# Kernel optimization log

Hardware: AMD Instinct MI355X
Metric: run time of the kernel (lower is better)

## Reference

```python
import jax, jax.numpy as jnp
import numpy as np

DEPTH = 4      # number of VSS blocks
C = 256        # channels / d_inner (expansion_factor=1)
DS = 16        # d_state
DTR = 16       # dt_rank = ceil(C/16)
BATCH, DD, HH, WW = 2, 16, 16, 16


def _ln(x, g, b, eps=1e-5):
    m = jnp.mean(x, -1, keepdims=True)
    v = jnp.var(x, -1, keepdims=True)
    return (x - m) * jax.lax.rsqrt(v + eps) * g + b


def _silu(x):
    return x * jax.nn.sigmoid(x)


def _block(x, ori, p):
    # x: [B,H,W,Dp,C] channel-last volume tokens
    B, H, W, Dp, Cd = x.shape
    L = H * W * Dp
    h = _ln(x, p['ln1_g'], p['ln1_b'])
    xz = h @ p['in_w'].T                       # [B,H,W,Dp,2C]
    xs, z = jnp.split(xz, 2, axis=-1)
    xc = jnp.transpose(xs, (0, 4, 1, 2, 3))    # [B,C,H,W,Dp]
    xc = jax.lax.conv_general_dilated(
        xc, p['conv_w'], (1, 1, 1), 'SAME',
        dimension_numbers=('NCDHW', 'OIDHW', 'NCDHW'),
        feature_group_count=Cd) + p['conv_b'][None, :, None, None, None]
    xc = _silu(xc)
    # orientation: 3 bits flip the spatial axes before raster flatten
    flip_axes = tuple(ax for bit, ax in ((1, 2), (2, 3), (4, 4)) if ori & bit)
    if flip_axes:
        xc = jnp.flip(xc, flip_axes)
    seq = xc.reshape(B, Cd, L).transpose(0, 2, 1)   # [B,L,C]
    dbl = seq @ p['xproj_w'].T                       # [B,L,DTR+2*DS]
    dt, Bm, Cm = dbl[..., :DTR], dbl[..., DTR:DTR + DS], dbl[..., DTR + DS:]
    dt = jax.nn.softplus(dt @ p['dt_w'].T + p['dt_b'])   # [B,L,C]
    A = -jnp.exp(p['A_log'])                              # [C,DS]
    dA = jnp.exp(dt[..., None] * A)                       # [B,L,C,DS]
    dBx = dt[..., None] * Bm[:, :, None, :] * seq[..., None]

    def step(carry, inp):
        dA_t, dBx_t, C_t = inp
        carry = dA_t * carry + dBx_t                      # [B,C,DS]
        y = jnp.einsum('bdn,bn->bd', carry, C_t)
        return carry, y

    h0 = jnp.zeros((B, Cd, DS), dA.dtype)
    _, ys = jax.lax.scan(step, h0, (dA.transpose(1, 0, 2, 3),
                                    dBx.transpose(1, 0, 2, 3),
                                    Cm.transpose(1, 0, 2)))
    y = ys.transpose(1, 0, 2) + p['D'] * seq              # [B,L,C]
    yv = y.transpose(0, 2, 1).reshape(B, Cd, H, W, Dp)
    if flip_axes:
        yv = jnp.flip(yv, flip_axes)
    y = jnp.transpose(yv, (0, 2, 3, 4, 1))                # [B,H,W,Dp,C]
    y = _ln(y, p['on_g'], p['on_b'])
    y = y * _silu(z)
    return x + y @ p['out_w'].T


def setup_inputs() -> dict:
    key = jax.random.key(0)
    ks = jax.random.split(key, 12)
    d = {}
    d['x'] = jax.random.normal(ks[0], (BATCH, C, DD, HH, WW), jnp.float32)
    d['in_w'] = jax.random.normal(ks[1], (DEPTH, 2 * C, C), jnp.float32) * 0.02
    d['conv_w'] = jax.random.normal(ks[2], (DEPTH, C, 1, 3, 3, 3), jnp.float32) * 0.1
    d['conv_b'] = jnp.zeros((DEPTH, C), jnp.float32)
    d['xproj_w'] = jax.random.normal(ks[3], (DEPTH, DTR + 2 * DS, C), jnp.float32) * 0.02
    d['dt_w'] = jax.random.normal(ks[4], (DEPTH, C, DTR), jnp.float32) * 0.02
    d['dt_b'] = jax.random.uniform(ks[5], (DEPTH, C), jnp.float32, -4.0, -2.0)
    # S4D-real init for A_log
    d['A_log'] = jnp.tile(jnp.log(jnp.arange(1, DS + 1, dtype=jnp.float32))[None, None, :], (DEPTH, C, 1))
    d['D_skip'] = jnp.ones((DEPTH, C), jnp.float32)
    d['on_g'] = jnp.ones((DEPTH, C), jnp.float32)
    d['on_b'] = jnp.zeros((DEPTH, C), jnp.float32)
    d['out_w'] = jax.random.normal(ks[6], (DEPTH, C, C), jnp.float32) * 0.02
    d['ln1_g'] = jnp.ones((DEPTH, C), jnp.float32)
    d['ln1_b'] = jnp.zeros((DEPTH, C), jnp.float32)
    d['post_g'] = jnp.ones((C,), jnp.float32)
    d['post_b'] = jnp.zeros((C,), jnp.float32)
    return d


def reference(x, in_w, conv_w, conv_b, xproj_w, dt_w, dt_b, A_log, D_skip,
              on_g, on_b, out_w, ln1_g, ln1_b, post_g, post_b):
    # [B,C,D,H,W] -> [B,H,W,D,C]
    t = jnp.transpose(x, (0, 3, 4, 2, 1))
    for i in range(DEPTH):
        p = dict(in_w=in_w[i], conv_w=conv_w[i], conv_b=conv_b[i],
                 xproj_w=xproj_w[i], dt_w=dt_w[i], dt_b=dt_b[i],
                 A_log=A_log[i], D=D_skip[i], on_g=on_g[i], on_b=on_b[i],
                 out_w=out_w[i], ln1_g=ln1_g[i], ln1_b=ln1_b[i])
        t = _block(t, i % 8, p)
    t = _ln(t, post_g, post_b)
    # [B,H,W,D,C] -> [B,C,D,H,W]
    return jnp.transpose(t, (0, 4, 3, 1, 2))
```

## Files before the change

kernel.cpp:

```cpp
#include <hip/hip_runtime.h>
#include <math.h>

#define B_ 2
#define C_ 256
#define L_ 4096
#define BL_ 8192
#define DEPTH_ 4
#define CK_ 64
#define CL_ 64

typedef __attribute__((ext_vector_type(8))) short bf16x8;
typedef __attribute__((ext_vector_type(4))) float f32x4;
#define MFMA16 __builtin_amdgcn_mfma_f32_16x16x32_bf16

__device__ __forceinline__ float silu_(float x){ return x/(1.f+__expf(-x)); }
__device__ __forceinline__ float softplus_(float x){ return fmaxf(x,0.f)+log1pf(__expf(-fabsf(x))); }
__device__ __forceinline__ unsigned short f2b_(float f){
    union{float f;unsigned u;}v; v.f=f;
    unsigned r=(v.u + 0x7fffu + ((v.u>>16)&1u))>>16;
    return (unsigned short)r;
}
__device__ __forceinline__ float b2f_(unsigned short u){
    union{unsigned u;float f;}v; v.u=((unsigned)u)<<16; return v.f;
}

__global__ __launch_bounds__(256) void k_w2b(const float* __restrict__ src, unsigned short* __restrict__ dst)
{
    int i=blockIdx.x*256+threadIdx.x;
    float4 v=((const float4*)src)[i];
    ushort4 o; o.x=f2b_(v.x); o.y=f2b_(v.y); o.z=f2b_(v.z); o.w=f2b_(v.w);
    ((ushort4*)dst)[i]=o;
}

__global__ __launch_bounds__(256) void k_wdt(
    const float* __restrict__ dtw, const float* __restrict__ xw,
    unsigned short* __restrict__ wdtb)
{
    int blk=blockIdx.x;
    int i=blk>>8, c=blk&255, k=threadIdx.x;
    const float* dr=dtw+((size_t)i*C_+c)*16;
    const float* xr=xw+(size_t)i*48*C_+k;
    float acc=0.f;
    #pragma unroll
    for(int j=0;j<16;j++) acc=fmaf(dr[j], xr[(size_t)j*C_], acc);
    wdtb[((size_t)i*C_+c)*C_+k]=f2b_(acc);
}

__global__ __launch_bounds__(256) void k_t_in(const float* __restrict__ x, float* __restrict__ t)
{
    __shared__ float tile[16*257];
    int blk=blockIdx.x, b=blk>>8, d=(blk>>4)&15, h=blk&15;
    int tid=threadIdx.x;
    int w2=tid&15;
    for(int p=0;p<16;p++){
        int c=(tid>>4)+16*p;
        tile[w2*257+c]=x[((size_t)(b*C_+c))*4096 + d*256 + h*16 + w2];
    }
    __syncthreads();
    for(int k=0;k<16;k++){
        t[((size_t)b*L_+(h*16+k)*16+d)*C_+tid]=tile[k*257+tid];
    }
}

__global__ __launch_bounds__(256) void k_ln(
    const float* __restrict__ t, const float* __restrict__ g,
    const float* __restrict__ be, unsigned short* __restrict__ hb)
{
    int wv=threadIdx.x>>6, lane=threadIdx.x&63;
    int row=blockIdx.x*4+wv;
    float4 v=((const float4*)(t+(size_t)row*C_))[lane];
    float s=v.x+v.y+v.z+v.w;
    float ss=v.x*v.x+v.y*v.y+v.z*v.z+v.w*v.w;
    #pragma unroll
    for(int m=1;m<64;m<<=1){ s+=__shfl_xor(s,m); ss+=__shfl_xor(ss,m); }
    float mn=s*(1.f/256.f);
    float rs=rsqrtf(ss*(1.f/256.f)-mn*mn+1e-5f);
    float4 gg=((const float4*)g)[lane];
    float4 bb=((const float4*)be)[lane];
    ushort4 o;
    o.x=f2b_((v.x-mn)*rs*gg.x+bb.x);
    o.y=f2b_((v.y-mn)*rs*gg.y+bb.y);
    o.z=f2b_((v.z-mn)*rs*gg.z+bb.z);
    o.w=f2b_((v.w-mn)*rs*gg.w+bb.w);
    ((ushort4*)(hb+(size_t)row*C_))[lane]=o;
}

__global__ __launch_bounds__(256) void k_gemm_in(
    const unsigned short* __restrict__ Ab, const unsigned short* __restrict__ Wb,
    float* __restrict__ xs, float* __restrict__ z)
{
    int wv=threadIdx.x>>6, lane=threadIdx.x&63;
    int m0=blockIdx.x*64+(wv>>1)*32;
    int n0=blockIdx.y*64+(wv&1)*32;
    int la=lane&15, kg=lane>>4;
    f32x4 acc[2][2];
    #pragma unroll
    for(int i=0;i<2;i++)
        #pragma unroll
        for(int j=0;j<2;j++) acc[i][j]=(f32x4){0.f,0.f,0.f,0.f};
    const unsigned short* a0p=Ab+(size_t)(m0+la)*C_+kg*8;
    const unsigned short* a1p=Ab+(size_t)(m0+16+la)*C_+kg*8;
    const unsigned short* b0p=Wb+(size_t)(n0+la)*C_+kg*8;
    const unsigned short* b1p=Wb+(size_t)(n0+16+la)*C_+kg*8;
    #pragma unroll
    for(int kk=0;kk<C_;kk+=32){
        bf16x8 a0=*(const bf16x8*)(a0p+kk);
        bf16x8 a1=*(const bf16x8*)(a1p+kk);
        bf16x8 b0=*(const bf16x8*)(b0p+kk);
        bf16x8 b1=*(const bf16x8*)(b1p+kk);
        acc[0][0]=MFMA16(a0,b0,acc[0][0],0,0,0);
        acc[0][1]=MFMA16(a0,b1,acc[0][1],0,0,0);
        acc[1][0]=MFMA16(a1,b0,acc[1][0],0,0,0);
        acc[1][1]=MFMA16(a1,b1,acc[1][1],0,0,0);
    }
    #pragma unroll
    for(int mi=0;mi<2;mi++)
        #pragma unroll
        for(int nj=0;nj<2;nj++)
            #pragma unroll
            for(int r=0;r<4;r++){
                int m=m0+mi*16+kg*4+r;
                int n=n0+nj*16+la;
                float val=acc[mi][nj][r];
                if(n<256) xs[(size_t)m*C_+n]=val;
                else      z [(size_t)m*C_+(n-256)]=val;
            }
}

__global__ __launch_bounds__(256) void k_gemm_out(
    const unsigned short* __restrict__ Ab, const unsigned short* __restrict__ Wb,
    float* __restrict__ t)
{
    int wv=threadIdx.x>>6, lane=threadIdx.x&63;
    int m0=blockIdx.x*64+(wv>>1)*32;
    int n0=blockIdx.y*64+(wv&1)*32;
    int la=lane&15, kg=lane>>4;
    f32x4 acc[2][2];
    #pragma unroll
    for(int i=0;i<2;i++)
        #pragma unroll
        for(int j=0;j<2;j++) acc[i][j]=(f32x4){0.f,0.f,0.f,0.f};
    const unsigned short* a0p=Ab+(size_t)(m0+la)*C_+kg*8;
    const unsigned short* a1p=Ab+(size_t)(m0+16+la)*C_+kg*8;
    const unsigned short* b0p=Wb+(size_t)(n0+la)*C_+kg*8;
    const unsigned short* b1p=Wb+(size_t)(n0+16+la)*C_+kg*8;
    #pragma unroll
    for(int kk=0;kk<C_;kk+=32){
        bf16x8 a0=*(const bf16x8*)(a0p+kk);
        bf16x8 a1=*(const bf16x8*)(a1p+kk);
        bf16x8 b0=*(const bf16x8*)(b0p+kk);
        bf16x8 b1=*(const bf16x8*)(b1p+kk);
        acc[0][0]=MFMA16(a0,b0,acc[0][0],0,0,0);
        acc[0][1]=MFMA16(a0,b1,acc[0][1],0,0,0);
        acc[1][0]=MFMA16(a1,b0,acc[1][0],0,0,0);
        acc[1][1]=MFMA16(a1,b1,acc[1][1],0,0,0);
    }
    #pragma unroll
    for(int mi=0;mi<2;mi++)
        #pragma unroll
        for(int nj=0;nj<2;nj++)
            #pragma unroll
            for(int r=0;r<4;r++){
                int m=m0+mi*16+kg*4+r;
                int n=n0+nj*16+la;
                float* tp=t+(size_t)m*C_+n;
                *tp=*tp+acc[mi][nj][r];
            }
}

__global__ __launch_bounds__(256) void k_gemm_xdt(
    const unsigned short* __restrict__ Ab, const unsigned short* __restrict__ Wxb,
    const unsigned short* __restrict__ Wdtb, const float* __restrict__ dtbias,
    float* __restrict__ BC, float* __restrict__ dt)
{
    int by=blockIdx.y;
    int wv=threadIdx.x>>6, lane=threadIdx.x&63;
    int la=lane&15, kg=lane>>4;
    f32x4 acc[2][2];
    #pragma unroll
    for(int i=0;i<2;i++)
        #pragma unroll
        for(int j=0;j<2;j++) acc[i][j]=(f32x4){0.f,0.f,0.f,0.f};
    if(by==4){
        if(blockIdx.x>=64) return;
        int m0=blockIdx.x*128+wv*32;
        const unsigned short* a0p=Ab+(size_t)(m0+la)*C_+kg*8;
        const unsigned short* a1p=Ab+(size_t)(m0+16+la)*C_+kg*8;
        const unsigned short* b0p=Wxb+(size_t)(16+la)*C_+kg*8;
        const unsigned short* b1p=Wxb+(size_t)(32+la)*C_+kg*8;
        #pragma unroll
        for(int kk=0;kk<C_;kk+=32){
            bf16x8 a0=*(const bf16x8*)(a0p+kk);
            bf16x8 a1=*(const bf16x8*)(a1p+kk);
            bf16x8 b0=*(const bf16x8*)(b0p+kk);
            bf16x8 b1=*(const bf16x8*)(b1p+kk);
            acc[0][0]=MFMA16(a0,b0,acc[0][0],0,0,0);
            acc[0][1]=MFMA16(a0,b1,acc[0][1],0,0,0);
            acc[1][0]=MFMA16(a1,b0,acc[1][0],0,0,0);
            acc[1][1]=MFMA16(a1,b1,acc[1][1],0,0,0);
        }
        #pragma unroll
        for(int mi=0;mi<2;mi++)
            #pragma unroll
            for(int nj=0;nj<2;nj++)
                #pragma unroll
                for(int r=0;r<4;r++){
                    int m=m0+mi*16+kg*4+r;
                    BC[(size_t)m*32 + nj*16+la]=acc[mi][nj][r];
                }
    } else {
        int m0=blockIdx.x*64+(wv>>1)*32;
        int n0=by*64+(wv&1)*32;
        const unsigned short* a0p=Ab+(size_t)(m0+la)*C_+kg*8;
        const unsigned short* a1p=Ab+(size_t)(m0+16+la)*C_+kg*8;
        const unsigned short* b0p=Wdtb+(size_t)(n0+la)*C_+kg*8;
        const unsigned short* b1p=Wdtb+(size_t)(n0+16+la)*C_+kg*8;
        #pragma unroll
        for(int kk=0;kk<C_;kk+=32){
            bf16x8 a0=*(const bf16x8*)(a0p+kk);
            bf16x8 a1=*(const bf16x8*)(a1p+kk);
            bf16x8 b0=*(const bf16x8*)(b0p+kk);
            bf16x8 b1=*(const bf16x8*)(b1p+kk);
            acc[0][0]=MFMA16(a0,b0,acc[0][0],0,0,0);
            acc[0][1]=MFMA16(a0,b1,acc[0][1],0,0,0);
            acc[1][0]=MFMA16(a1,b0,acc[1][0],0,0,0);
            acc[1][1]=MFMA16(a1,b1,acc[1][1],0,0,0);
        }
        float bias0=dtbias[n0+la], bias1=dtbias[n0+16+la];
        #pragma unroll
        for(int mi=0;mi<2;mi++)
            #pragma unroll
            for(int nj=0;nj<2;nj++)
                #pragma unroll
                for(int r=0;r<4;r++){
                    int m=m0+mi*16+kg*4+r;
                    int n=n0+nj*16+la;
                    float val=acc[mi][nj][r]+((nj==0)?bias0:bias1);
                    dt[(size_t)m*C_+n]=softplus_(val);
                }
    }
}

__global__ __launch_bounds__(256) void k_conv(
    const float* __restrict__ xs, const float* __restrict__ cw,
    const float* __restrict__ cb, unsigned short* __restrict__ seqb, int ori)
{
    __shared__ float wl[256*27];
    int tid=threadIdx.x;
    for(int j=tid;j<256*27;j+=256) wl[j]=cw[j];
    int blk=blockIdx.x;
    int b=blk>>8, h=(blk>>4)&15, w=blk&15;
    __syncthreads();
    const float* wp=wl+tid*27;
    float bias=cb[tid];
    float acc[16];
    #pragma unroll
    for(int d=0;d<16;d++) acc[d]=bias;
    #pragma unroll
    for(int kh=0;kh<3;kh++){
        int hh=h+kh-1; if((unsigned)hh>=16u) continue;
        #pragma unroll
        for(int kw=0;kw<3;kw++){
            int ww=w+kw-1; if((unsigned)ww>=16u) continue;
            const float* bp=xs+((size_t)(b*L_)+(hh*16+ww)*16)*C_+tid;
            float w0=wp[(kh*3+kw)*3+0];
            float w1=wp[(kh*3+kw)*3+1];
            float w2=wp[(kh*3+kw)*3+2];
            #pragma unroll
            for(int dd=0;dd<16;dd++){
                float v=bp[(size_t)dd*C_];
                if(dd<15) acc[dd+1]=fmaf(w0,v,acc[dd+1]);
                acc[dd]=fmaf(w1,v,acc[dd]);
                if(dd>0)  acc[dd-1]=fmaf(w2,v,acc[dd-1]);
            }
        }
    }
    int hf=(ori&1)?15-h:h;
    int wf=(ori&2)?15-w:w;
    size_t obase=((size_t)b*L_+(hf*16+wf)*16)*C_+tid;
    #pragma unroll
    for(int d=0;d<16;d++){
        float a=silu_(acc[d]);
        int df=(ori&4)?15-d:d;
        seqb[obase+(size_t)df*C_]=f2b_(a);
    }
}

__global__ __launch_bounds__(256) void k_scan1(
    const unsigned short* __restrict__ seqb, const float* __restrict__ dtlc,
    const float* __restrict__ BC, const float* __restrict__ A_log,
    float* __restrict__ Ap, float* __restrict__ Ho)
{
    __shared__ float2 dxL[64][17];
    __shared__ float  bcL[64][16];
    int tid=threadIdx.x;
    int blk=blockIdx.x, cg=blk>>6, ck=blk&63;
    int p0=cg*16, b=p0>>8, c0=p0&255;
    int l0=ck*CL_;
    {
        int lr=tid>>2, c4=tid&3;
        size_t base=((size_t)(b*L_+l0+lr))*C_ + c0 + c4*4;
        ushort4 xu=*(const ushort4*)(seqb+base);
        float4 d4=*(const float4*)(dtlc+base);
        dxL[lr][c4*4+0]=make_float2(d4.x,b2f_(xu.x));
        dxL[lr][c4*4+1]=make_float2(d4.y,b2f_(xu.y));
        dxL[lr][c4*4+2]=make_float2(d4.z,b2f_(xu.z));
        dxL[lr][c4*4+3]=make_float2(d4.w,b2f_(xu.w));
        if(c4==0){
            const float* bs=BC+((size_t)(b*L_+l0+lr))*32;
            float4 bv0=*(const float4*)bs, bv1=*(const float4*)(bs+4);
            float4 bv2=*(const float4*)(bs+8), bv3=*(const float4*)(bs+12);
            *(float4*)&bcL[lr][0]=bv0;  *(float4*)&bcL[lr][4]=bv1;
            *(float4*)&bcL[lr][8]=bv2;  *(float4*)&bcL[lr][12]=bv3;
        }
    }
    __syncthreads();
    int wv=tid>>6, lane=tid&63, grp=lane>>4, n=lane&15;
    int cl=wv*4+grp, pair=p0+cl, c=c0+cl;
    float An=-__expf(A_log[c*16+n]);
    float carry=0.f, sdt=0.f;
    #pragma unroll 8
    for(int l=0;l<CL_;l++){
        float2 dx=dxL[l][cl];
        float bv=bcL[l][n];
        float dA=__expf(dx.x*An);
        carry=fmaf(dA,carry,dx.x*bv*dx.y);
        sdt+=dx.x;
    }
    int idx=(pair*CK_+ck)*16+n;
    Ap[idx]=__expf(An*sdt); Ho[idx]=carry;
}

__global__ __launch_bounds__(256) void k_scan2(
    const float* __restrict__ Ap, const float* __restrict__ Ho, float* __restrict__ Sb)
{
    int gid=blockIdx.x*256+threadIdx.x;
    int pair=gid>>4, n=gid&15;
    float S=0.f;
    #pragma unroll
    for(int ck=0;ck<CK_;ck++){
        int idx=(pair*CK_+ck)*16+n;
        Sb[idx]=S;
        S=fmaf(Ap[idx],S,Ho[idx]);
    }
}

__global__ __launch_bounds__(256) void k_scan3(
    const unsigned short* __restrict__ seqb, const float* __restrict__ dtlc,
    const float* __restrict__ BC, const float* __restrict__ A_log,
    const float* __restrict__ Dsk, const float* __restrict__ Sb,
    float* __restrict__ y)
{
    __shared__ float2 dxL[64][17];
    __shared__ float  bcL[64][32];
    __shared__ float  sc[16][16][17];
    int tid=threadIdx.x;
    int blk=blockIdx.x, cg=blk>>6, ck=blk&63;
    int p0=cg*16, b=p0>>8, c0=p0&255;
    int l0=ck*CL_;
    {
        int lr=tid>>2, c4=tid&3;
        size_t base=((size_t)(b*L_+l0+lr))*C_ + c0 + c4*4;
        ushort4 xu=*(const ushort4*)(seqb+base);
        float4 d4=*(const float4*)(dtlc+base);
        dxL[lr][c4*4+0]=make_float2(d4.x,b2f_(xu.x));
        dxL[lr][c4*4+1]=make_float2(d4.y,b2f_(xu.y));
        dxL[lr][c4*4+2]=make_float2(d4.z,b2f_(xu.z));
        dxL[lr][c4*4+3]=make_float2(d4.w,b2f_(xu.w));
        const float* bs=BC+((size_t)(b*L_+l0+lr))*32 + c4*8;
        float4 bv0=*(const float4*)bs, bv1=*(const float4*)(bs+4);
        *(float4*)&bcL[lr][c4*8]=bv0;
        *(float4*)&bcL[lr][c4*8+4]=bv1;
    }
    __syncthreads();
    int wv=tid>>6, lane=tid&63, grp=lane>>4, n=lane&15;
    int cl=wv*4+grp, pair=p0+cl, c=c0+cl;
    float An=-__expf(A_log[c*16+n]);
    float Dc=Dsk[c];
    float carry=Sb[(pair*CK_+ck)*16+n];
    float ybuf[4], xsv[4];
    #pragma unroll
    for(int q=0;q<4;q++){
        float parts[16];
        #pragma unroll
        for(int l2=0;l2<16;l2++){
            int l=q*16+l2;
            float2 dx=dxL[l][cl];
            float bv=bcL[l][n];
            float cv=bcL[l][16+n];
            float dA=__expf(dx.x*An);
            carry=fmaf(dA,carry,dx.x*bv*dx.y);
            parts[l2]=carry*cv;
            if(l2==n) xsv[q]=dx.y;
        }
        #pragma unroll
        for(int l2=0;l2<16;l2++) sc[cl][l2][n]=parts[l2];
        __syncthreads();
        float s=0.f;
        #pragma unroll
        for(int n2=0;n2<16;n2++) s+=sc[cl][n][n2];
        ybuf[q]=fmaf(Dc,xsv[q],s);
        __syncthreads();
    }
    float* yT=(float*)&sc[0][0][0];
    #pragma unroll
    for(int q=0;q<4;q++){
        int l=q*16+n;
        yT[l*17+cl]=ybuf[q];
    }
    __syncthreads();
    {
        int lr=tid>>2, c4=tid&3;
        size_t base=((size_t)(b*L_+l0+lr))*C_ + c0 + c4*4;
        float4 o=make_float4(yT[lr*17+c4*4+0],yT[lr*17+c4*4+1],
                             yT[lr*17+c4*4+2],yT[lr*17+c4*4+3]);
        *(float4*)(y+base)=o;
    }
}

__global__ __launch_bounds__(256) void k_post(
    const float* __restrict__ y, const float* __restrict__ z,
    const float* __restrict__ og, const float* __restrict__ ob,
    unsigned short* __restrict__ y2b, int ori)
{
    int wv=threadIdx.x>>6, lane=threadIdx.x&63;
    int row=blockIdx.x*4+wv;
    int b=row>>12, l=row&4095;
    int d=l&15, w=(l>>4)&15, h=l>>8;
    int hf=(ori&1)?15-h:h, wf=(ori&2)?15-w:w, df=(ori&4)?15-d:d;
    int lf=(hf*16+wf)*16+df;
    float4 v=((const float4*)(y+((size_t)b*L_+lf)*C_))[lane];
    float s=v.x+v.y+v.z+v.w;
    float ss=v.x*v.x+v.y*v.y+v.z*v.z+v.w*v.w;
    #pragma unroll
    for(int m=1;m<64;m<<=1){ s+=__shfl_xor(s,m); ss+=__shfl_xor(ss,m); }
    float mn=s*(1.f/256.f);
    float rstd=rsqrtf(ss*(1.f/256.f)-mn*mn+1e-5f);
    float4 gg=((const float4*)og)[lane];
    float4 bb=((const float4*)ob)[lane];
    float4 zv=((const float4*)(z+((size_t)b*L_+l)*C_))[lane];
    ushort4 o;
    o.x=f2b_(((v.x-mn)*rstd*gg.x+bb.x)*silu_(zv.x));
    o.y=f2b_(((v.y-mn)*rstd*gg.y+bb.y)*silu_(zv.y));
    o.z=f2b_(((v.z-mn)*rstd*gg.z+bb.z)*silu_(zv.z));
    o.w=f2b_(((v.w-mn)*rstd*gg.w+bb.w)*silu_(zv.w));
    ((ushort4*)(y2b+((size_t)b*L_+l)*C_))[lane]=o;
}

__global__ __launch_bounds__(256) void k_final(
    const float* __restrict__ t, const float* __restrict__ pg,
    const float* __restrict__ pb, float* __restrict__ out)
{
    __shared__ float tile[16*257];
    __shared__ float mrs[16][2];
    int blk=blockIdx.x, b=blk>>8, d=(blk>>4)&15, h=blk&15;
    int tid=threadIdx.x;
    for(int w2=0;w2<16;w2++){
        tile[w2*257+tid]=t[((size_t)b*L_+(h*16+w2)*16+d)*C_+tid];
    }
    __syncthreads();
    int r=tid>>4, p=tid&15;
    float s=0.f, ss=0.f;
    #pragma unroll
    for(int k=0;k<16;k++){ float v=tile[r*257+k*16+p]; s+=v; ss+=v*v; }
    #pragma unroll
    for(int m=1;m<16;m<<=1){ s+=__shfl_xor(s,m); ss+=__shfl_xor(ss,m); }
    if(p==0){ float mn=s*(1.f/256.f); mrs[r][0]=mn; mrs[r][1]=rsqrtf(ss*(1.f/256.f)-mn*mn+1e-5f); }
    __syncthreads();
    int w2=tid&15;
    for(int p2=0;p2<16;p2++){
        int c=(tid>>4)+16*p2;
        float v=tile[w2*257+c];
        float vn=(v-mrs[w2][0])*mrs[w2][1]*pg[c]+pb[c];
        out[((size_t)(b*C_+c))*4096 + d*256 + h*16 + w2]=vn;
    }
}

extern "C" void kernel_launch(void* const* d_in, const int* in_sizes, int n_in,
                              void* d_out, int out_size, void* d_ws, size_t ws_size,
                              hipStream_t stream)
{
    (void)in_sizes; (void)n_in; (void)out_size; (void)ws_size;
    const float* x      =(const float*)d_in[0];
    const float* in_w   =(const float*)d_in[1];
    const float* conv_w =(const float*)d_in[2];
    const float* conv_b =(const float*)d_in[3];
    const float* xproj_w=(const float*)d_in[4];
    const float* dt_w   =(const float*)d_in[5];
    const float* dt_b   =(const float*)d_in[6];
    const float* A_log  =(const float*)d_in[7];
    const float* D_skip =(const float*)d_in[8];
    const float* on_g   =(const float*)d_in[9];
    const float* on_b   =(const float*)d_in[10];
    const float* out_w  =(const float*)d_in[11];
    const float* ln1_g  =(const float*)d_in[12];
    const float* ln1_b  =(const float*)d_in[13];
    const float* post_g =(const float*)d_in[14];
    const float* post_b =(const float*)d_in[15];
    float* out=(float*)d_out;
    float* ws=(float*)d_ws;

    const size_t NBL=(size_t)BL_*C_;
    float* t    = ws;
    float* xs   = ws +   NBL;
    float* z    = ws + 2*NBL;
    float* seq  = ws + 3*NBL;
    float* BC   = ws + 4*NBL;
    float* Ap   = BC + (size_t)BL_*32;
    float* Ho   = Ap + 512*CK_*16;
    float* Sb   = Ho + 512*CK_*16;
    unsigned short* hb   = (unsigned short*)(Sb + 512*CK_*16);
    unsigned short* seqb = hb   + NBL;
    unsigned short* y2b  = seqb + NBL;
    unsigned short* wbI  = y2b  + NBL;
    unsigned short* wbO  = wbI + (size_t)DEPTH_*512*C_;
    unsigned short* xwb  = wbO + (size_t)DEPTH_*C_*C_;
    unsigned short* wdtb = xwb + (size_t)DEPTH_*48*C_;
    float* dtlc = xs;

    k_w2b<<<DEPTH_*512*C_/1024,256,0,stream>>>(in_w, wbI);
    k_w2b<<<DEPTH_*C_*C_/1024,256,0,stream>>>(out_w, wbO);
    k_w2b<<<DEPTH_*48*C_/1024,256,0,stream>>>(xproj_w, xwb);
    k_wdt<<<DEPTH_*C_,256,0,stream>>>(dt_w, xproj_w, wdtb);
    k_t_in<<<512,256,0,stream>>>(x,t);
    for(int i=0;i<DEPTH_;i++){
        int ori=i&7;
        k_ln<<<2048,256,0,stream>>>(t, ln1_g+i*256, ln1_b+i*256, hb);
        k_gemm_in<<<dim3(128,8),256,0,stream>>>(hb, wbI+(size_t)i*512*C_, xs, z);
        k_conv<<<512,256,0,stream>>>(xs, conv_w+(size_t)i*6912, conv_b+i*256, seqb, ori);
        k_gemm_xdt<<<dim3(128,5),256,0,stream>>>(seqb, xwb+(size_t)i*48*C_, wdtb+(size_t)i*C_*C_, dt_b+i*256, BC, dtlc);
        k_scan1<<<2048,256,0,stream>>>(seqb, dtlc, BC, A_log+(size_t)i*4096, Ap, Ho);
        k_scan2<<<32,256,0,stream>>>(Ap, Ho, Sb);
        k_scan3<<<2048,256,0,stream>>>(seqb, dtlc, BC, A_log+(size_t)i*4096, D_skip+i*256, Sb, seq);
        k_post<<<2048,256,0,stream>>>(seq, z, on_g+i*256, on_b+i*256, y2b, ori);
        k_gemm_out<<<dim3(128,4),256,0,stream>>>(y2b, wbO+(size_t)i*C_*C_, t);
    }
    k_final<<<512,256,0,stream>>>(t, post_g, post_b, out);
}
```

Measured before the change: 508.8 us.

## Fuse layernorm into input GEMM and post-norm into output GEMM, merge prep kernels

Computes the LayerNorm of each 64-row tile directly into shared memory inside the input-projection GEMM, and the gated output-norm inside the output-projection GEMM. This removes the bf16 intermediate buffers and two launches per block. The four weight-conversion kernels are merged into one launch. The cost is that each norm is now recomputed by every N-tile block (8x and 4x redundancy), and each block does serial LN work before its MFMA loop starts.

New measurement: 481.2 us. 5.4% less time.

```diff
diff --git a/kernel.cpp b/kernel.cpp
--- a/kernel.cpp
+++ b/kernel.cpp
@@ -24,26 +24,38 @@
     union{unsigned u;float f;}v; v.u=((unsigned)u)<<16; return v.f;
 }
 
-__global__ __launch_bounds__(256) void k_w2b(const float* __restrict__ src, unsigned short* __restrict__ dst)
-{
-    int i=blockIdx.x*256+threadIdx.x;
-    float4 v=((const float4*)src)[i];
-    ushort4 o; o.x=f2b_(v.x); o.y=f2b_(v.y); o.z=f2b_(v.z); o.w=f2b_(v.w);
-    ((ushort4*)dst)[i]=o;
-}
-
-__global__ __launch_bounds__(256) void k_wdt(
-    const float* __restrict__ dtw, const float* __restrict__ xw,
-    unsigned short* __restrict__ wdtb)
-{
-    int blk=blockIdx.x;
-    int i=blk>>8, c=blk&255, k=threadIdx.x;
-    const float* dr=dtw+((size_t)i*C_+c)*16;
-    const float* xr=xw+(size_t)i*48*C_+k;
-    float acc=0.f;
-    #pragma unroll
-    for(int j=0;j<16;j++) acc=fmaf(dr[j], xr[(size_t)j*C_], acc);
-    wdtb[((size_t)i*C_+c)*C_+k]=f2b_(acc);
+__global__ __launch_bounds__(256) void k_prep(
+    const float* __restrict__ in_w, const float* __restrict__ out_w,
+    const float* __restrict__ xproj_w, const float* __restrict__ dtw,
+    unsigned short* __restrict__ wbI, unsigned short* __restrict__ wbO,
+    unsigned short* __restrict__ xwb, unsigned short* __restrict__ wdtb)
+{
+    int bid=blockIdx.x, tid=threadIdx.x;
+    if(bid<512){
+        int i=bid*256+tid;
+        float4 v=((const float4*)in_w)[i];
+        ushort4 o; o.x=f2b_(v.x); o.y=f2b_(v.y); o.z=f2b_(v.z); o.w=f2b_(v.w);
+        ((ushort4*)wbI)[i]=o;
+    } else if(bid<768){
+        int i=(bid-512)*256+tid;
+        float4 v=((const float4*)out_w)[i];
+        ushort4 o; o.x=f2b_(v.x); o.y=f2b_(v.y); o.z=f2b_(v.z); o.w=f2b_(v.w);
+        ((ushort4*)wbO)[i]=o;
+    } else if(bid<816){
+        int i=(bid-768)*256+tid;
+        float4 v=((const float4*)xproj_w)[i];
+        ushort4 o; o.x=f2b_(v.x); o.y=f2b_(v.y); o.z=f2b_(v.z); o.w=f2b_(v.w);
+        ((ushort4*)xwb)[i]=o;
+    } else {
+        int blk=bid-816;
+        int i=blk>>8, c=blk&255, k=tid;
+        const float* dr=dtw+((size_t)i*C_+c)*16;
+        const float* xr=xproj_w+(size_t)i*48*C_+k;
+        float acc=0.f;
+        #pragma unroll
+        for(int j=0;j<16;j++) acc=fmaf(dr[j], xr[(size_t)j*C_], acc);
+        wdtb[((size_t)i*C_+c)*C_+k]=f2b_(acc);
+    }
 }
 
 __global__ __launch_bounds__(256) void k_t_in(const float* __restrict__ x, float* __restrict__ t)
@@ -62,50 +74,47 @@
     }
 }
 
-__global__ __launch_bounds__(256) void k_ln(
+__global__ __launch_bounds__(256) void k_ln_gemm_in(
     const float* __restrict__ t, const float* __restrict__ g,
-    const float* __restrict__ be, unsigned short* __restrict__ hb)
-{
-    int wv=threadIdx.x>>6, lane=threadIdx.x&63;
-    int row=blockIdx.x*4+wv;
-    float4 v=((const float4*)(t+(size_t)row*C_))[lane];
-    float s=v.x+v.y+v.z+v.w;
-    float ss=v.x*v.x+v.y*v.y+v.z*v.z+v.w*v.w;
-    #pragma unroll
-    for(int m=1;m<64;m<<=1){ s+=__shfl_xor(s,m); ss+=__shfl_xor(ss,m); }
-    float mn=s*(1.f/256.f);
-    float rs=rsqrtf(ss*(1.f/256.f)-mn*mn+1e-5f);
+    const float* __restrict__ be, const unsigned short* __restrict__ Wb,
+    float* __restrict__ xs, float* __restrict__ z)
+{
+    __shared__ unsigned short A[64][264];
+    int tid=threadIdx.x, wv=tid>>6, lane=tid&63;
+    int m0=blockIdx.x*64, n0=blockIdx.y*64;
     float4 gg=((const float4*)g)[lane];
     float4 bb=((const float4*)be)[lane];
-    ushort4 o;
-    o.x=f2b_((v.x-mn)*rs*gg.x+bb.x);
-    o.y=f2b_((v.y-mn)*rs*gg.y+bb.y);
-    o.z=f2b_((v.z-mn)*rs*gg.z+bb.z);
-    o.w=f2b_((v.w-mn)*rs*gg.w+bb.w);
-    ((ushort4*)(hb+(size_t)row*C_))[lane]=o;
-}
-
-__global__ __launch_bounds__(256) void k_gemm_in(
-    const unsigned short* __restrict__ Ab, const unsigned short* __restrict__ Wb,
-    float* __restrict__ xs, float* __restrict__ z)
-{
-    int wv=threadIdx.x>>6, lane=threadIdx.x&63;
-    int m0=blockIdx.x*64+(wv>>1)*32;
-    int n0=blockIdx.y*64+(wv&1)*32;
+    #pragma unroll 4
+    for(int i=0;i<16;i++){
+        int row=wv*16+i;
+        float4 v=((const float4*)(t+(size_t)(m0+row)*C_))[lane];
+        float s=v.x+v.y+v.z+v.w;
+        float ss=v.x*v.x+v.y*v.y+v.z*v.z+v.w*v.w;
+        #pragma unroll
+        for(int m=1;m<64;m<<=1){ s+=__shfl_xor(s,m); ss+=__shfl_xor(ss,m); }
+        float mn=s*(1.f/256.f);
+        float rs=rsqrtf(ss*(1.f/256.f)-mn*mn+1e-5f);
+        ushort4 o;
+        o.x=f2b_((v.x-mn)*rs*gg.x+bb.x);
+        o.y=f2b_((v.y-mn)*rs*gg.y+bb.y);
+        o.z=f2b_((v.z-mn)*rs*gg.z+bb.z);
+        o.w=f2b_((v.w-mn)*rs*gg.w+bb.w);
+        *(ushort4*)&A[row][lane*4]=o;
+    }
+    __syncthreads();
     int la=lane&15, kg=lane>>4;
+    int mh=(wv>>1)*32, nh=n0+(wv&1)*32;
     f32x4 acc[2][2];
     #pragma unroll
     for(int i=0;i<2;i++)
         #pragma unroll
         for(int j=0;j<2;j++) acc[i][j]=(f32x4){0.f,0.f,0.f,0.f};
-    const unsigned short* a0p=Ab+(size_t)(m0+la)*C_+kg*8;
-    const unsigned short* a1p=Ab+(size_t)(m0+16+la)*C_+kg*8;
-    const unsigned short* b0p=Wb+(size_t)(n0+la)*C_+kg*8;
-    const unsigned short* b1p=Wb+(size_t)(n0+16+la)*C_+kg*8;
+    const unsigned short* b0p=Wb+(size_t)(nh+la)*C_+kg*8;
+    const unsigned short* b1p=Wb+(size_t)(nh+16+la)*C_+kg*8;
     #pragma unroll
     for(int kk=0;kk<C_;kk+=32){
-        bf16x8 a0=*(const bf16x8*)(a0p+kk);
-        bf16x8 a1=*(const bf16x8*)(a1p+kk);
+        bf16x8 a0=*(const bf16x8*)&A[mh+la][kg*8+kk];
+        bf16x8 a1=*(const bf16x8*)&A[mh+16+la][kg*8+kk];
         bf16x8 b0=*(const bf16x8*)(b0p+kk);
         bf16x8 b1=*(const bf16x8*)(b1p+kk);
         acc[0][0]=MFMA16(a0,b0,acc[0][0],0,0,0);
@@ -119,35 +128,61 @@
         for(int nj=0;nj<2;nj++)
             #pragma unroll
             for(int r=0;r<4;r++){
-                int m=m0+mi*16+kg*4+r;
-                int n=n0+nj*16+la;
+                int m=m0+mh+mi*16+kg*4+r;
+                int n=nh+nj*16+la;
                 float val=acc[mi][nj][r];
                 if(n<256) xs[(size_t)m*C_+n]=val;
                 else      z [(size_t)m*C_+(n-256)]=val;
             }
 }
 
-__global__ __launch_bounds__(256) void k_gemm_out(
-    const unsigned short* __restrict__ Ab, const unsigned short* __restrict__ Wb,
-    float* __restrict__ t)
-{
-    int wv=threadIdx.x>>6, lane=threadIdx.x&63;
-    int m0=blockIdx.x*64+(wv>>1)*32;
-    int n0=blockIdx.y*64+(wv&1)*32;
+__global__ __launch_bounds__(256) void k_post_gemm_out(
+    const float* __restrict__ y, const float* __restrict__ z,
+    const float* __restrict__ og, const float* __restrict__ ob,
+    const unsigned short* __restrict__ Wb, float* __restrict__ t, int ori)
+{
+    __shared__ unsigned short A[64][264];
+    int tid=threadIdx.x, wv=tid>>6, lane=tid&63;
+    int m0=blockIdx.x*64, n0=blockIdx.y*64;
+    float4 gg=((const float4*)og)[lane];
+    float4 bb=((const float4*)ob)[lane];
+    #pragma unroll 4
+    for(int i=0;i<16;i++){
+        int row=wv*16+i;
+        int rm=m0+row;
+        int b=rm>>12, l=rm&4095;
+        int d=l&15, w=(l>>4)&15, h=l>>8;
+        int hf=(ori&1)?15-h:h, wf=(ori&2)?15-w:w, df=(ori&4)?15-d:d;
+        int lf=(hf*16+wf)*16+df;
+        float4 v=((const float4*)(y+((size_t)b*L_+lf)*C_))[lane];
+        float s=v.x+v.y+v.z+v.w;
+        float ss=v.x*v.x+v.y*v.y+v.z*v.z+v.w*v.w;
+        #pragma unroll
+        for(int m=1;m<64;m<<=1){ s+=__shfl_xor(s,m); ss+=__shfl_xor(ss,m); }
+        float mn=s*(1.f/256.f);
+        float rstd=rsqrtf(ss*(1.f/256.f)-mn*mn+1e-5f);
+        float4 zv=((const float4*)(z+((size_t)b*L_+l)*C_))[lane];
+        ushort4 o;
+        o.x=f2b_(((v.x-mn)*rstd*gg.x+bb.x)*silu_(zv.x));
+        o.y=f2b_(((v.y-mn)*rstd*gg.y+bb.y)*silu_(zv.y));
+        o.z=f2b_(((v.z-mn)*rstd*gg.z+bb.z)*silu_(zv.z));
+        o.w=f2b_(((v.w-mn)*rstd*gg.w+bb.w)*silu_(zv.w));
+        *(ushort4*)&A[row][lane*4]=o;
+    }
+    __syncthreads();
     int la=lane&15, kg=lane>>4;
+    int mh=(wv>>1)*32, nh=n0+(wv&1)*32;
     f32x4 acc[2][2];
     #pragma unroll
     for(int i=0;i<2;i++)
         #pragma unroll
         for(int j=0;j<2;j++) acc[i][j]=(f32x4){0.f,0.f,0.f,0.f};
-    const unsigned short* a0p=Ab+(size_t)(m0+la)*C_+kg*8;
-    const unsigned short* a1p=Ab+(size_t)(m0+16+la)*C_+kg*8;
-    const unsigned short* b0p=Wb+(size_t)(n0+la)*C_+kg*8;
-    const unsigned short* b1p=Wb+(size_t)(n0+16+la)*C_+kg*8;
+    const unsigned short* b0p=Wb+(size_t)(nh+la)*C_+kg*8;
+    const unsigned short* b1p=Wb+(size_t)(nh+16+la)*C_+kg*8;
     #pragma unroll
     for(int kk=0;kk<C_;kk+=32){
-        bf16x8 a0=*(const bf16x8*)(a0p+kk);
-        bf16x8 a1=*(const bf16x8*)(a1p+kk);
+        bf16x8 a0=*(const bf16x8*)&A[mh+la][kg*8+kk];
+        bf16x8 a1=*(const bf16x8*)&A[mh+16+la][kg*8+kk];
         bf16x8 b0=*(const bf16x8*)(b0p+kk);
         bf16x8 b1=*(const bf16x8*)(b1p+kk);
         acc[0][0]=MFMA16(a0,b0,acc[0][0],0,0,0);
@@ -161,8 +196,8 @@
         for(int nj=0;nj<2;nj++)
             #pragma unroll
             for(int r=0;r<4;r++){
-                int m=m0+mi*16+kg*4+r;
-                int n=n0+nj*16+la;
+                int m=m0+mh+mi*16+kg*4+r;
+                int n=nh+nj*16+la;
                 float* tp=t+(size_t)m*C_+n;
                 *tp=*tp+acc[mi][nj][r];
             }
@@ -418,35 +453,6 @@
     }
 }
 
-__global__ __launch_bounds__(256) void k_post(
-    const float* __restrict__ y, const float* __restrict__ z,
-    const float* __restrict__ og, const float* __restrict__ ob,
-    unsigned short* __restrict__ y2b, int ori)
-{
-    int wv=threadIdx.x>>6, lane=threadIdx.x&63;
-    int row=blockIdx.x*4+wv;
-    int b=row>>12, l=row&4095;
-    int d=l&15, w=(l>>4)&15, h=l>>8;
-    int hf=(ori&1)?15-h:h, wf=(ori&2)?15-w:w, df=(ori&4)?15-d:d;
-    int lf=(hf*16+wf)*16+df;
-    float4 v=((const float4*)(y+((size_t)b*L_+lf)*C_))[lane];
-    float s=v.x+v.y+v.z+v.w;
-    float ss=v.x*v.x+v.y*v.y+v.z*v.z+v.w*v.w;
-    #pragma unroll
-    for(int m=1;m<64;m<<=1){ s+=__shfl_xor(s,m); ss+=__shfl_xor(ss,m); }
-    float mn=s*(1.f/256.f);
-    float rstd=rsqrtf(ss*(1.f/256.f)-mn*mn+1e-5f);
-    float4 gg=((const float4*)og)[lane];
-    float4 bb=((const float4*)ob)[lane];
-    float4 zv=((const float4*)(z+((size_t)b*L_+l)*C_))[lane];
-    ushort4 o;
-    o.x=f2b_(((v.x-mn)*rstd*gg.x+bb.x)*silu_(zv.x));
-    o.y=f2b_(((v.y-mn)*rstd*gg.y+bb.y)*silu_(zv.y));
-    o.z=f2b_(((v.z-mn)*rstd*gg.z+bb.z)*silu_(zv.z));
-    o.w=f2b_(((v.w-mn)*rstd*gg.w+bb.w)*silu_(zv.w));
-    ((ushort4*)(y2b+((size_t)b*L_+l)*C_))[lane]=o;
-}
-
 __global__ __launch_bounds__(256) void k_final(
     const float* __restrict__ t, const float* __restrict__ pg,
     const float* __restrict__ pb, float* __restrict__ out)
@@ -509,31 +515,24 @@
     float* Ap   = BC + (size_t)BL_*32;
     float* Ho   = Ap + 512*CK_*16;
     float* Sb   = Ho + 512*CK_*16;
-    unsigned short* hb   = (unsigned short*)(Sb + 512*CK_*16);
-    unsigned short* seqb = hb   + NBL;
-    unsigned short* y2b  = seqb + NBL;
-    unsigned short* wbI  = y2b  + NBL;
+    unsigned short* seqb = (unsigned short*)(Sb + 512*CK_*16);
+    unsigned short* wbI  = seqb + NBL;
     unsigned short* wbO  = wbI + (size_t)DEPTH_*512*C_;
     unsigned short* xwb  = wbO + (size_t)DEPTH_*C_*C_;
     unsigned short* wdtb = xwb + (size_t)DEPTH_*48*C_;
     float* dtlc = xs;
 
-    k_w2b<<<DEPTH_*512*C_/1024,256,0,stream>>>(in_w, wbI);
-    k_w2b<<<DEPTH_*C_*C_/1024,256,0,stream>>>(out_w, wbO);
-    k_w2b<<<DEPTH_*48*C_/1024,256,0,stream>>>(xproj_w, xwb);
-    k_wdt<<<DEPTH_*C_,256,0,stream>>>(dt_w, xproj_w, wdtb);
+    k_prep<<<1840,256,0,stream>>>(in_w, out_w, xproj_w, dt_w, wbI, wbO, xwb, wdtb);
     k_t_in<<<512,256,0,stream>>>(x,t);
     for(int i=0;i<DEPTH_;i++){
         int ori=i&7;
-        k_ln<<<2048,256,0,stream>>>(t, ln1_g+i*256, ln1_b+i*256, hb);
-        k_gemm_in<<<dim3(128,8),256,0,stream>>>(hb, wbI+(size_t)i*512*C_, xs, z);
+        k_ln_gemm_in<<<dim3(128,8),256,0,stream>>>(t, ln1_g+i*256, ln1_b+i*256, wbI+(size_t)i*512*C_, xs, z);
         k_conv<<<512,256,0,stream>>>(xs, conv_w+(size_t)i*6912, conv_b+i*256, seqb, ori);
         k_gemm_xdt<<<dim3(128,5),256,0,stream>>>(seqb, xwb+(size_t)i*48*C_, wdtb+(size_t)i*C_*C_, dt_b+i*256, BC, dtlc);
         k_scan1<<<2048,256,0,stream>>>(seqb, dtlc, BC, A_log+(size_t)i*4096, Ap, Ho);
         k_scan2<<<32,256,0,stream>>>(Ap, Ho, Sb);
         k_scan3<<<2048,256,0,stream>>>(seqb, dtlc, BC, A_log+(size_t)i*4096, D_skip+i*256, Sb, seq);
-        k_post<<<2048,256,0,stream>>>(seq, z, on_g+i*256, on_b+i*256, y2b, ori);
-        k_gemm_out<<<dim3(128,4),256,0,stream>>>(y2b, wbO+(size_t)i*C_*C_, t);
+        k_post_gemm_out<<<dim3(128,4),256,0,stream>>>(seq, z, on_g+i*256, on_b+i*256, wbO+(size_t)i*C_*C_, t, ori);
     }
     k_final<<<512,256,0,stream>>>(t, post_g, post_b, out);
 }
```
